# Optimization experiments

Measured on AMD Instinct MI355X. Metric: run time of the kernel, lower is better.

Reference implementation:

```python
import jax, jax.numpy as jnp
import numpy as np

T = 5
V_TH = 0.5
GAMMA = 0.5
W_DECAY = 0.5
LOWER = 0.2 - 0.03
UPPER = 0.2 + 0.03
EMA_INIT = 0.17

@jax.custom_vjp
def sg_heaviside(x):
    return (x >= 0).astype(x.dtype)

def _sg_fwd(x):
    return sg_heaviside(x), x

def _sg_bwd(x, g):
    # grad_output * clamp(gamma - |x|, 0) / gamma^2  (triangular surrogate)
    return (g * jnp.clip(GAMMA - jnp.abs(x), 0.0) / (GAMMA * GAMMA),)

sg_heaviside.defvjp(_sg_fwd, _sg_bwd)


def setup_inputs() -> dict:
    key = jax.random.key(0)
    k1, k2 = jax.random.split(key)
    shape = (T, 32, 128, 32, 32)  # [T, B, C, H, W]
    x_exc = jax.random.uniform(k1, shape, dtype=jnp.float32)
    x_inh = jax.random.uniform(k2, shape, dtype=jnp.float32)
    alpha_raw = jnp.zeros((), dtype=jnp.float32)  # nn.Parameter alpha init 0.0
    beta_raw = jnp.zeros((), dtype=jnp.float32)   # nn.Parameter beta init 0.0
    return {"x_exc": x_exc, "x_inh": x_inh, "alpha_raw": alpha_raw, "beta_raw": beta_raw}


def reference(x_exc, x_inh, alpha_raw, beta_raw):
    beta = jax.nn.sigmoid(beta_raw)
    alpha = 4.0 * jax.nn.sigmoid(alpha_raw)
    B, C, H, W = x_exc.shape[1:]
    mem0 = jnp.zeros((B, C, H, W), x_exc.dtype)
    # ema starts constant 0.17 full-shape; after first mean it is [1,C,1,1].
    # Starting with [1,C,1,1] constant is mathematically identical.
    ema0 = jnp.full((1, C, 1, 1), EMA_INIT, x_exc.dtype)
    inhw0 = jnp.zeros((1, C, 1, 1), x_exc.dtype)

    def step(carry, xs):
        mem, ema, inhw = carry
        xe, xi = xs
        e_input = xe / (1.0 + alpha * xi)
        mem = W_DECAY * mem + e_input - beta * xi * (1.0 - inhw)
        spike = sg_heaviside(mem - V_TH)
        # ema update uses detached spikes; broadcasts [1,C,1,1]+[B,C,H,W] then means back
        ema = jnp.mean(0.9 * ema + 0.1 * jax.lax.stop_gradient(spike),
                       axis=(0, 2, 3), keepdims=True)
        # original only updates inh_weight for t < T-1, but the last update is
        # never read, so updating unconditionally is equivalent
        inhw = 4.0 * (jax.nn.sigmoid(LOWER - ema) - jax.nn.sigmoid(ema - UPPER))
        mem = mem - V_TH * spike
        return (mem, ema, inhw), spike

    _, spikes = jax.lax.scan(step, (mem0, ema0, inhw0), (x_exc, x_inh))
    return spikes  # [T, B, C, H, W]
```

## Files before the change

### kernel.cpp

```cpp
#include <hip/hip_runtime.h>

constexpr int T    = 5;
constexpr int C    = 128;
constexpr int NPT4 = 32 * C * 1024 / 4;

constexpr int SBLOCKS  = 1024;
constexpr int STHREADS = 256;
constexpr int KT       = 4;

constexpr size_t PART_BYTES = (size_t)T * SBLOCKS * sizeof(unsigned int);
constexpr size_t WS_NEEDED  = PART_BYTES + (size_t)NPT4 * 16;

__global__ __launch_bounds__(STHREADS)
void lif_step(const float4* __restrict__ xe4,
              const float4* __restrict__ xi4,
              const float* __restrict__ alpha_raw,
              const float* __restrict__ beta_raw,
              float4* __restrict__ out4,
              float4* __restrict__ memb,
              unsigned int* __restrict__ partials,
              int t) {
#pragma clang fp contract(off)
  const int blk = blockIdx.x;
  const int tid = threadIdx.x;
  const int c   = blk & (C - 1);

  __shared__ float s_inhw;
  if (tid == 0) {
    float inhw = 0.0f;
    if (t > 0) {
      float ema = 0.17f;
      for (int s = 0; s < t; ++s) {
        unsigned int tot = 0;
#pragma unroll
        for (int i = 0; i < 8; ++i) tot += partials[s * SBLOCKS + c + i * C];
        const float mean = (float)tot * (1.0f / 32768.0f);
        ema = 0.9f * ema + 0.1f * mean;
      }
      const float s_lo = 1.0f / (1.0f + expf(-(0.17f - ema)));
      const float s_hi = 1.0f / (1.0f + expf(-(ema - 0.23f)));
      inhw = 4.0f * (s_lo - s_hi);
    }
    s_inhw = inhw;
  }
  __syncthreads();
  const float inhw  = s_inhw;
  const float alpha = 4.0f / (1.0f + expf(-alpha_raw[0]));
  const float beta  = 1.0f / (1.0f + expf(-beta_raw[0]));

  unsigned int local = 0;
  const size_t tb = (size_t)t * NPT4;
#pragma unroll
  for (int k = 0; k < KT; ++k) {
    const size_t fi = (size_t)(k * SBLOCKS + blk) * 256 + tid;
    const float4 e4 = xe4[tb + fi];
    const float4 i4 = xi4[tb + fi];
    float4 m4 = {0.0f, 0.0f, 0.0f, 0.0f};
    if (t > 0) m4 = memb[fi];
    const float xe[4] = {e4.x, e4.y, e4.z, e4.w};
    const float xi[4] = {i4.x, i4.y, i4.z, i4.w};
    float mv[4] = {m4.x, m4.y, m4.z, m4.w};
    float sv[4];
#pragma unroll
    for (int j = 0; j < 4; ++j) {
      const float e_in = xe[j] / (1.0f + alpha * xi[j]);
      const float a  = 0.5f * mv[j];
      const float bb = a + e_in;
      const float d  = (beta * xi[j]) * (1.0f - inhw);
      const float m  = bb - d;
      const float x  = m - 0.5f;
      const float s  = (x >= 0.0f) ? 1.0f : 0.0f;
      local += (x >= 0.0f) ? 1u : 0u;
      mv[j] = m - 0.5f * s;
      sv[j] = s;
    }
    float4 s4; s4.x = sv[0]; s4.y = sv[1]; s4.z = sv[2]; s4.w = sv[3];
    out4[tb + fi] = s4;
    if (t < T - 1) {
      float4 nm; nm.x = mv[0]; nm.y = mv[1]; nm.z = mv[2]; nm.w = mv[3];
      memb[fi] = nm;
    }
  }

  if (t < T - 1) {
#pragma unroll
    for (int off = 32; off > 0; off >>= 1) local += __shfl_down(local, off);
    __shared__ unsigned int wsum[STHREADS / 64];
    if ((tid & 63) == 0) wsum[tid >> 6] = local;
    __syncthreads();
    if (tid == 0)
      partials[t * SBLOCKS + blk] = wsum[0] + wsum[1] + wsum[2] + wsum[3];
  }
}

constexpr int FTHREADS = 1024;
constexpr int FWAVES   = FTHREADS / 64;
constexpr int FBLOCKS  = 2 * C;
constexpr int FK       = 8;

__global__ __launch_bounds__(FTHREADS)
void lif_fallback(const float* __restrict__ xe_g, const float* __restrict__ xi_g,
                  const float* __restrict__ alpha_raw,
                  const float* __restrict__ beta_raw, float* __restrict__ out) {
#pragma clang fp contract(off)
  const int blk = blockIdx.x, c = blk & (C - 1), half = blk >> 7;
  const int tid = threadIdx.x, wave = tid >> 6, lane = tid & 63;
  __shared__ unsigned int wsum[T - 1][FWAVES];
  const float alpha = 4.0f / (1.0f + expf(-alpha_raw[0]));
  const float beta  = 1.0f / (1.0f + expf(-beta_raw[0]));
  float mem[FK][4];
#pragma unroll
  for (int k = 0; k < FK; ++k)
#pragma unroll
    for (int j = 0; j < 4; ++j) mem[k][j] = 0.0f;
  float ema = 0.17f, inhw = 0.0f;
  const float4* xe4 = (const float4*)xe_g;
  const float4* xi4 = (const float4*)xi_g;
  float4* o4 = (float4*)out;
  auto gidx = [&](int t, int k) -> size_t {
    const int b = k * (FTHREADS / 256) + (tid >> 8);
    return (size_t)t * NPT4 + (size_t)(b * C + c) * 256 + (tid & 255);
  };
  for (int t = 0; t < T; ++t) {
    float4 e4[FK], i4[FK];
#pragma unroll
    for (int k = 0; k < FK; ++k) { const size_t idx = gidx(t, k); e4[k] = xe4[idx]; i4[k] = xi4[idx]; }
    unsigned int local = 0;
#pragma unroll
    for (int k = 0; k < FK; ++k) {
      const float xe[4] = {e4[k].x, e4[k].y, e4[k].z, e4[k].w};
      const float xi[4] = {i4[k].x, i4[k].y, i4[k].z, i4[k].w};
      float sv[4];
#pragma unroll
      for (int j = 0; j < 4; ++j) {
        const float e_in = xe[j] / (1.0f + alpha * xi[j]);
        const float a = 0.5f * mem[k][j];
        const float bb = a + e_in;
        const float d = (beta * xi[j]) * (1.0f - inhw);
        const float m = bb - d;
        const float x = m - 0.5f;
        const float s = (x >= 0.0f) ? 1.0f : 0.0f;
        local += (x >= 0.0f) ? 1u : 0u;
        mem[k][j] = m - 0.5f * s;
        sv[j] = s;
      }
      if ((k >> 2) == half) {
        float4 s4; s4.x = sv[0]; s4.y = sv[1]; s4.z = sv[2]; s4.w = sv[3];
        o4[gidx(t, k)] = s4;
      }
    }
    if (t == T - 1) break;
#pragma unroll
    for (int off = 32; off > 0; off >>= 1) local += __shfl_down(local, off);
    if (lane == 0) wsum[t][wave] = local;
    __syncthreads();
    unsigned int total = 0;
#pragma unroll
    for (int w = 0; w < FWAVES; ++w) total += wsum[t][w];
    const float mean_spike = (float)total * (1.0f / 32768.0f);
    ema = 0.9f * ema + 0.1f * mean_spike;
    const float s_lo = 1.0f / (1.0f + expf(-(0.17f - ema)));
    const float s_hi = 1.0f / (1.0f + expf(-(ema - 0.23f)));
    inhw = 4.0f * (s_lo - s_hi);
  }
}

extern "C" void kernel_launch(void* const* d_in, const int* in_sizes, int n_in,
                              void* d_out, int out_size, void* d_ws, size_t ws_size,
                              hipStream_t stream) {
  const float* xe = (const float*)d_in[0];
  const float* xi = (const float*)d_in[1];
  const float* ar = (const float*)d_in[2];
  const float* br = (const float*)d_in[3];
  float* out = (float*)d_out;

  if (ws_size >= WS_NEEDED) {
    unsigned int* partials = (unsigned int*)d_ws;
    float4* memb = (float4*)((char*)d_ws + PART_BYTES);
    const float4* xe4 = (const float4*)xe;
    const float4* xi4 = (const float4*)xi;
    float4* out4 = (float4*)out;
    for (int t = 0; t < T; ++t)
      lif_step<<<dim3(SBLOCKS), dim3(STHREADS), 0, stream>>>(
          xe4, xi4, ar, br, out4, memb, partials, t);
  } else {
    lif_fallback<<<dim3(FBLOCKS), dim3(FTHREADS), 0, stream>>>(xe, xi, ar, br, out);
  }
}
```

Measured before the change: 227.8 us.

## Fuse timestep launches into one cooperative kernel with grid sync

Replaces the five per-timestep launches with a single cooperative kernel. Membrane state stays in registers across timesteps, and a grid-wide sync exchanges per-channel spike counts between steps. This removes the global read and write of the membrane buffer and the launch overhead of each step. Loads for the next timestep are issued before the current step's compute and the grid barrier, to overlap memory latency. It depends on all 1024 blocks being co-resident, and each grid sync costs a barrier.

```diff
diff --git a/kernel.cpp b/kernel.cpp
--- a/kernel.cpp
+++ b/kernel.cpp
@@ -1,4 +1,7 @@
 #include <hip/hip_runtime.h>
+#include <hip/hip_cooperative_groups.h>
+
+namespace cg = cooperative_groups;
 
 constexpr int T    = 5;
 constexpr int C    = 128;
@@ -10,6 +13,113 @@
 
 constexpr size_t PART_BYTES = (size_t)T * SBLOCKS * sizeof(unsigned int);
 constexpr size_t WS_NEEDED  = PART_BYTES + (size_t)NPT4 * 16;
+
+__global__ __launch_bounds__(STHREADS, 4)
+void lif_coop(const float4* __restrict__ xe4,
+              const float4* __restrict__ xi4,
+              const float* __restrict__ alpha_raw,
+              const float* __restrict__ beta_raw,
+              float4* __restrict__ out4,
+              unsigned int* __restrict__ partials) {
+#pragma clang fp contract(off)
+  const int blk = blockIdx.x;
+  const int tid = threadIdx.x;
+  const int c   = blk & (C - 1);
+  __shared__ float s_inhw;
+  __shared__ unsigned int wsum[STHREADS / 64];
+
+  const float alpha = 4.0f / (1.0f + expf(-alpha_raw[0]));
+  const float beta  = 1.0f / (1.0f + expf(-beta_raw[0]));
+
+  const size_t fi0 = (size_t)blk * 256 + tid;
+
+  float4 e[KT], i[KT], en[KT], ix[KT];
+#pragma unroll
+  for (int k = 0; k < KT; ++k) {
+    const size_t fi = fi0 + (size_t)(k * SBLOCKS) * 256;
+    e[k] = xe4[fi];
+    i[k] = xi4[fi];
+  }
+
+  float mv[KT][4];
+#pragma unroll
+  for (int k = 0; k < KT; ++k)
+#pragma unroll
+    for (int j = 0; j < 4; ++j) mv[k][j] = 0.0f;
+
+  float inhw = 0.0f;
+  float ema  = 0.17f;
+  cg::grid_group grid = cg::this_grid();
+
+  for (int t = 0; t < T; ++t) {
+    const size_t tb = (size_t)t * NPT4;
+
+    if (t < T - 1) {
+      const size_t tb1 = tb + NPT4;
+#pragma unroll
+      for (int k = 0; k < KT; ++k) {
+        const size_t fi = fi0 + (size_t)(k * SBLOCKS) * 256;
+        en[k] = xe4[tb1 + fi];
+        ix[k] = xi4[tb1 + fi];
+      }
+    }
+
+    unsigned int local = 0;
+#pragma unroll
+    for (int k = 0; k < KT; ++k) {
+      const size_t fi = fi0 + (size_t)(k * SBLOCKS) * 256;
+      const float xe[4] = {e[k].x, e[k].y, e[k].z, e[k].w};
+      const float xi[4] = {i[k].x, i[k].y, i[k].z, i[k].w};
+      float sv[4];
+#pragma unroll
+      for (int j = 0; j < 4; ++j) {
+        const float e_in = xe[j] / (1.0f + alpha * xi[j]);
+        const float a  = 0.5f * mv[k][j];
+        const float bb = a + e_in;
+        const float d  = (beta * xi[j]) * (1.0f - inhw);
+        const float m  = bb - d;
+        const float x  = m - 0.5f;
+        const float s  = (x >= 0.0f) ? 1.0f : 0.0f;
+        local += (x >= 0.0f) ? 1u : 0u;
+        mv[k][j] = m - 0.5f * s;
+        sv[j] = s;
+      }
+      float4 s4; s4.x = sv[0]; s4.y = sv[1]; s4.z = sv[2]; s4.w = sv[3];
+      out4[tb + fi] = s4;
+    }
+    if (t == T - 1) break;
+
+#pragma unroll
+    for (int off = 32; off > 0; off >>= 1) local += __shfl_down(local, off);
+    if ((tid & 63) == 0) wsum[tid >> 6] = local;
+    __syncthreads();
+    if (tid == 0) {
+      const unsigned int total = wsum[0] + wsum[1] + wsum[2] + wsum[3];
+      __hip_atomic_store(&partials[t * SBLOCKS + blk], total,
+                         __ATOMIC_RELEASE, __HIP_MEMORY_SCOPE_AGENT);
+    }
+
+    grid.sync();
+
+    if (tid == 0) {
+      unsigned int tot = 0;
+#pragma unroll
+      for (int q = 0; q < 8; ++q)
+        tot += __hip_atomic_load(&partials[t * SBLOCKS + c + q * C],
+                                 __ATOMIC_ACQUIRE, __HIP_MEMORY_SCOPE_AGENT);
+      const float mean = (float)tot * (1.0f / 32768.0f);
+      ema = 0.9f * ema + 0.1f * mean;
+      const float s_lo = 1.0f / (1.0f + expf(-(0.17f - ema)));
+      const float s_hi = 1.0f / (1.0f + expf(-(ema - 0.23f)));
+      s_inhw = 4.0f * (s_lo - s_hi);
+    }
+    __syncthreads();
+    inhw = s_inhw;
+
+#pragma unroll
+    for (int k = 0; k < KT; ++k) { e[k] = en[k]; i[k] = ix[k]; }
+  }
+}
 
 __global__ __launch_bounds__(STHREADS)
 void lif_step(const float4* __restrict__ xe4,
@@ -174,7 +284,37 @@
   const float* br = (const float*)d_in[3];
   float* out = (float*)d_out;
 
-  if (ws_size >= WS_NEEDED) {
+  static const int coop_ok = [] {
+    int dev = 0;
+    if (hipGetDevice(&dev) != hipSuccess) return 0;
+    int attr = 0;
+    if (hipDeviceGetAttribute(&attr, hipDeviceAttributeCooperativeLaunch, dev) != hipSuccess || !attr)
+      return 0;
+    int nb = 0;
+    if (hipOccupancyMaxActiveBlocksPerMultiprocessor(&nb, (const void*)lif_coop,
+                                                     STHREADS, 0) != hipSuccess)
+      return 0;
+    int cus = 0;
+    if (hipDeviceGetAttribute(&cus, hipDeviceAttributeMultiprocessorCount, dev) != hipSuccess)
+      return 0;
+    return (nb * cus >= SBLOCKS) ? 1 : 0;
+  }();
+
+  if (coop_ok && ws_size >= PART_BYTES) {
+    unsigned int* partials = (unsigned int*)d_ws;
+    const float4* xe4 = (const float4*)xe;
+    const float4* xi4 = (const float4*)xi;
+    float4* out4 = (float4*)out;
+    void* args[6];
+    args[0] = (void*)&xe4;
+    args[1] = (void*)&xi4;
+    args[2] = (void*)&ar;
+    args[3] = (void*)&br;
+    args[4] = (void*)&out4;
+    args[5] = (void*)&partials;
+    (void)hipLaunchCooperativeKernel((const void*)lif_coop, dim3(SBLOCKS),
+                                     dim3(STHREADS), args, 0, stream);
+  } else if (ws_size >= WS_NEEDED) {
     unsigned int* partials = (unsigned int*)d_ws;
     float4* memb = (float4*)((char*)d_ws + PART_BYTES);
     const float4* xe4 = (const float4*)xe;
```

New measurement: 226.9 us. About the same (-0.4%).

## Fuse per-timestep launches into one persistent kernel with atomic channel barriers

Applied to the files above, without the earlier changes.

Replaces the five per-timestep launches with a single kernel that keeps membrane state in registers across timesteps. Per-channel spike counts are exchanged through global atomic counters that pack an arrival count into the high bits, and each block spin-waits until all eight blocks of its channel have arrived. Next-timestep inputs are prefetched before the current step is computed. This removes the membrane-buffer round trip and the launch gaps, but it relies on all 1024 blocks being co-resident to avoid deadlock and adds an extra memset plus spin-wait latency.

```diff
diff --git a/kernel.cpp b/kernel.cpp
--- a/kernel.cpp
+++ b/kernel.cpp
@@ -8,88 +8,109 @@
 constexpr int STHREADS = 256;
 constexpr int KT       = 4;
 
-constexpr size_t PART_BYTES = (size_t)T * SBLOCKS * sizeof(unsigned int);
-constexpr size_t WS_NEEDED  = PART_BYTES + (size_t)NPT4 * 16;
-
-__global__ __launch_bounds__(STHREADS)
-void lif_step(const float4* __restrict__ xe4,
-              const float4* __restrict__ xi4,
-              const float* __restrict__ alpha_raw,
-              const float* __restrict__ beta_raw,
-              float4* __restrict__ out4,
-              float4* __restrict__ memb,
-              unsigned int* __restrict__ partials,
-              int t) {
+constexpr size_t ACC_BYTES = (size_t)T * C * sizeof(unsigned int);
+
+__global__ __launch_bounds__(STHREADS, 8)
+void lif_stream(const float4* __restrict__ xe4,
+                const float4* __restrict__ xi4,
+                const float* __restrict__ alpha_raw,
+                const float* __restrict__ beta_raw,
+                float4* __restrict__ out4,
+                unsigned int* __restrict__ acc) {
 #pragma clang fp contract(off)
   const int blk = blockIdx.x;
   const int tid = threadIdx.x;
   const int c   = blk & (C - 1);
-
   __shared__ float s_inhw;
-  if (tid == 0) {
-    float inhw = 0.0f;
-    if (t > 0) {
-      float ema = 0.17f;
-      for (int s = 0; s < t; ++s) {
-        unsigned int tot = 0;
-#pragma unroll
-        for (int i = 0; i < 8; ++i) tot += partials[s * SBLOCKS + c + i * C];
-        const float mean = (float)tot * (1.0f / 32768.0f);
-        ema = 0.9f * ema + 0.1f * mean;
-      }
+  __shared__ unsigned int wsum[STHREADS / 64];
+
+  const float alpha = 4.0f / (1.0f + expf(-alpha_raw[0]));
+  const float beta  = 1.0f / (1.0f + expf(-beta_raw[0]));
+
+  const size_t fi0 = (size_t)blk * 256 + tid;
+
+  float4 e[KT], i[KT], en[KT], ix[KT];
+#pragma unroll
+  for (int k = 0; k < KT; ++k) {
+    const size_t fi = fi0 + (size_t)(k * SBLOCKS) * 256;
+    e[k] = xe4[fi];
+    i[k] = xi4[fi];
+  }
+
+  float mv[KT][4];
+#pragma unroll
+  for (int k = 0; k < KT; ++k)
+#pragma unroll
+    for (int j = 0; j < 4; ++j) mv[k][j] = 0.0f;
+
+  float inhw = 0.0f;
+  float ema  = 0.17f;
+
+  for (int t = 0; t < T; ++t) {
+    const size_t tb = (size_t)t * NPT4;
+
+    if (t < T - 1) {
+      const size_t tb1 = tb + NPT4;
+#pragma unroll
+      for (int k = 0; k < KT; ++k) {
+        const size_t fi = fi0 + (size_t)(k * SBLOCKS) * 256;
+        en[k] = xe4[tb1 + fi];
+        ix[k] = xi4[tb1 + fi];
+      }
+    }
+
+    unsigned int local = 0;
+#pragma unroll
+    for (int k = 0; k < KT; ++k) {
+      const size_t fi = fi0 + (size_t)(k * SBLOCKS) * 256;
+      const float xe[4] = {e[k].x, e[k].y, e[k].z, e[k].w};
+      const float xi[4] = {i[k].x, i[k].y, i[k].z, i[k].w};
+      float sv[4];
+#pragma unroll
+      for (int j = 0; j < 4; ++j) {
+        const float e_in = xe[j] / (1.0f + alpha * xi[j]);
+        const float a  = 0.5f * mv[k][j];
+        const float bb = a + e_in;
+        const float d  = (beta * xi[j]) * (1.0f - inhw);
+        const float m  = bb - d;
+        const float x  = m - 0.5f;
+        const float s  = (x >= 0.0f) ? 1.0f : 0.0f;
+        local += (x >= 0.0f) ? 1u : 0u;
+        mv[k][j] = m - 0.5f * s;
+        sv[j] = s;
+      }
+      float4 s4; s4.x = sv[0]; s4.y = sv[1]; s4.z = sv[2]; s4.w = sv[3];
+      out4[tb + fi] = s4;
+    }
+    if (t == T - 1) break;
+
+#pragma unroll
+    for (int off = 32; off > 0; off >>= 1) local += __shfl_down(local, off);
+    if ((tid & 63) == 0) wsum[tid >> 6] = local;
+    __syncthreads();
+    if (tid == 0) {
+      const unsigned int total = wsum[0] + wsum[1] + wsum[2] + wsum[3];
+      unsigned int* cell = &acc[t * C + c];
+      __hip_atomic_fetch_add(cell, total | (1u << 28),
+                             __ATOMIC_RELEASE, __HIP_MEMORY_SCOPE_AGENT);
+      unsigned int v = __hip_atomic_load(cell, __ATOMIC_ACQUIRE,
+                                         __HIP_MEMORY_SCOPE_AGENT);
+      while ((v >> 28) < 8u) {
+        __builtin_amdgcn_s_sleep(2);
+        v = __hip_atomic_load(cell, __ATOMIC_ACQUIRE, __HIP_MEMORY_SCOPE_AGENT);
+      }
+      const unsigned int tot = v & 0x0FFFFFFFu;
+      const float mean = (float)tot * (1.0f / 32768.0f);
+      ema = 0.9f * ema + 0.1f * mean;
       const float s_lo = 1.0f / (1.0f + expf(-(0.17f - ema)));
       const float s_hi = 1.0f / (1.0f + expf(-(ema - 0.23f)));
-      inhw = 4.0f * (s_lo - s_hi);
-    }
-    s_inhw = inhw;
-  }
-  __syncthreads();
-  const float inhw  = s_inhw;
-  const float alpha = 4.0f / (1.0f + expf(-alpha_raw[0]));
-  const float beta  = 1.0f / (1.0f + expf(-beta_raw[0]));
-
-  unsigned int local = 0;
-  const size_t tb = (size_t)t * NPT4;
-#pragma unroll
-  for (int k = 0; k < KT; ++k) {
-    const size_t fi = (size_t)(k * SBLOCKS + blk) * 256 + tid;
-    const float4 e4 = xe4[tb + fi];
-    const float4 i4 = xi4[tb + fi];
-    float4 m4 = {0.0f, 0.0f, 0.0f, 0.0f};
-    if (t > 0) m4 = memb[fi];
-    const float xe[4] = {e4.x, e4.y, e4.z, e4.w};
-    const float xi[4] = {i4.x, i4.y, i4.z, i4.w};
-    float mv[4] = {m4.x, m4.y, m4.z, m4.w};
-    float sv[4];
-#pragma unroll
-    for (int j = 0; j < 4; ++j) {
-      const float e_in = xe[j] / (1.0f + alpha * xi[j]);
-      const float a  = 0.5f * mv[j];
-      const float bb = a + e_in;
-      const float d  = (beta * xi[j]) * (1.0f - inhw);
-      const float m  = bb - d;
-      const float x  = m - 0.5f;
-      const float s  = (x >= 0.0f) ? 1.0f : 0.0f;
-      local += (x >= 0.0f) ? 1u : 0u;
-      mv[j] = m - 0.5f * s;
-      sv[j] = s;
-    }
-    float4 s4; s4.x = sv[0]; s4.y = sv[1]; s4.z = sv[2]; s4.w = sv[3];
-    out4[tb + fi] = s4;
-    if (t < T - 1) {
-      float4 nm; nm.x = mv[0]; nm.y = mv[1]; nm.z = mv[2]; nm.w = mv[3];
-      memb[fi] = nm;
-    }
-  }
-
-  if (t < T - 1) {
-#pragma unroll
-    for (int off = 32; off > 0; off >>= 1) local += __shfl_down(local, off);
-    __shared__ unsigned int wsum[STHREADS / 64];
-    if ((tid & 63) == 0) wsum[tid >> 6] = local;
+      s_inhw = 4.0f * (s_lo - s_hi);
+    }
     __syncthreads();
-    if (tid == 0)
-      partials[t * SBLOCKS + blk] = wsum[0] + wsum[1] + wsum[2] + wsum[3];
+    inhw = s_inhw;
+
+#pragma unroll
+    for (int k = 0; k < KT; ++k) { e[k] = en[k]; i[k] = ix[k]; }
   }
 }
 
@@ -174,15 +195,14 @@
   const float* br = (const float*)d_in[3];
   float* out = (float*)d_out;
 
-  if (ws_size >= WS_NEEDED) {
-    unsigned int* partials = (unsigned int*)d_ws;
-    float4* memb = (float4*)((char*)d_ws + PART_BYTES);
+  if (ws_size >= ACC_BYTES) {
+    unsigned int* acc = (unsigned int*)d_ws;
     const float4* xe4 = (const float4*)xe;
     const float4* xi4 = (const float4*)xi;
     float4* out4 = (float4*)out;
-    for (int t = 0; t < T; ++t)
-      lif_step<<<dim3(SBLOCKS), dim3(STHREADS), 0, stream>>>(
-          xe4, xi4, ar, br, out4, memb, partials, t);
+    hipMemsetAsync(d_ws, 0, ACC_BYTES, stream);
+    lif_stream<<<dim3(SBLOCKS), dim3(STHREADS), 0, stream>>>(
+        xe4, xi4, ar, br, out4, acc);
   } else {
     lif_fallback<<<dim3(FBLOCKS), dim3(FTHREADS), 0, stream>>>(xe, xi, ar, br, out);
   }
```

Measured after the change: 505.0 us. +121.7%, slower.
